# Kernel tuning notes

Measured on AMD Instinct MI355X. Metric: run time of the kernel, lower is better.

The kernel has to match this reference:

```python
import jax, jax.numpy as jnp
import numpy as np

B = 16; Hp = 24; Wp = 24; N = Hp * Wp + 2  # 578 = patches + cls + freq tokens
D = 768; H = 12; HDIM = D // H
BAND = 64; SD = 16  # sd = min(16, max(4, band_dim))
HID = 3072  # int(embed_dim * mlp_ratio)
SCALE = HDIM ** -0.5; CLIP = 10.0
FILM_SCALE = 0.5; SPEC_INIT = 0.02; GATE_INIT = 0.05


def _ln(x, w, b, eps=1e-6):
    m = jnp.mean(x, axis=-1, keepdims=True)
    v = jnp.mean((x - m) ** 2, axis=-1, keepdims=True)
    return (x - m) * jax.lax.rsqrt(v + eps) * w + b


def _rms(x, eps=1e-6):
    return x * jax.lax.rsqrt(jnp.mean(x * x, axis=-1, keepdims=True) + eps)


def setup_inputs() -> dict:
    key = jax.random.key(0)
    ks = jax.random.split(key, 16)
    rn = lambda k, s, sc=1.0: jax.random.normal(k, s, dtype=jnp.float32) * sc
    return {
        "x": rn(ks[0], (B, N, D)),
        "band_tokens": rn(ks[1], (B, 1, D)),  # unused by forward (matches torch signature)
        "freq_token_for_cond": rn(ks[2], (B, 1, D)),
        "freq_summary": rn(ks[3], (B, D)),
        "token_band_feat": rn(ks[4], (B, N, BAND)),
        "alpha": jnp.ones((1,), jnp.float32),
        "ln_gate_w": jnp.ones((D,), jnp.float32), "ln_gate_b": jnp.zeros((D,), jnp.float32),
        "film_w": rn(ks[5], (D, 2 * D), 1e-4), "film_b": jnp.zeros((2 * D,), jnp.float32),
        "ln_attn_w": jnp.ones((D,), jnp.float32), "ln_attn_b": jnp.zeros((D,), jnp.float32),
        "qkv_w": rn(ks[6], (D, 3 * D), 0.02), "qkv_b": jnp.zeros((3 * D,), jnp.float32),
        "proj_w": rn(ks[7], (D, D), 0.02), "proj_b": jnp.zeros((D,), jnp.float32),
        "spec_bias_scale": jnp.float32(SPEC_INIT),
        "gate_w": rn(ks[8], (D, H), 1e-4), "gate_b": jnp.zeros((H,), jnp.float32),
        "band_proj_w": rn(ks[9], (BAND, SD), 0.02),
        "ln_mlp_w": jnp.ones((D,), jnp.float32), "ln_mlp_b": jnp.zeros((D,), jnp.float32),
        "fc1_w": rn(ks[10], (D, HID), 0.02), "fc1_b": jnp.zeros((HID,), jnp.float32),
        "fc2_w": rn(ks[11], (HID, D), 0.02), "fc2_b": jnp.zeros((D,), jnp.float32),
        "dw_w": rn(ks[12], (HID, 1, 3, 3), 0.1), "dw_b": jnp.zeros((HID,), jnp.float32),
    }


def _forward(x, band_tokens, freq_token_for_cond, freq_summary, token_band_feat, alpha,
             ln_gate_w, ln_gate_b, film_w, film_b, ln_attn_w, ln_attn_b,
             qkv_w, qkv_b, proj_w, proj_b, spec_bias_scale, gate_w, gate_b, band_proj_w,
             ln_mlp_w, ln_mlp_b, fc1_w, fc1_b, fc2_w, fc2_b, dw_w, dw_b):
    a = alpha.reshape(())
    # --- FiLM gate on patch tokens (replaces patch, no residual) ---
    cls_freq = x[:, :2]
    patch = x[:, 2:]
    p = _ln(patch, ln_gate_w, ln_gate_b)
    gb = freq_summary @ film_w + film_b            # [B, 2D]
    gamma, beta = jnp.split(gb, 2, axis=-1)
    gamma = jnp.tanh(gamma) * FILM_SCALE
    beta = jnp.tanh(beta) * FILM_SCALE
    patch = p * (1.0 + a * gamma[:, None, :]) + a * beta[:, None, :]
    x = jnp.concatenate([cls_freq, patch], axis=1)
    # --- spectral-similarity attention ---
    xn = _ln(x, ln_attn_w, ln_attn_b)
    qkv = (xn @ qkv_w + qkv_b).reshape(B, N, 3, H, HDIM)
    q = _rms(qkv[:, :, 0].transpose(0, 2, 1, 3))   # [B,H,N,hd]
    k = _rms(qkv[:, :, 1].transpose(0, 2, 1, 3))
    v = qkv[:, :, 2].transpose(0, 2, 1, 3)
    logits = jnp.einsum('bhnd,bhmd->bhnm', q * SCALE, k)
    s = _rms(token_band_feat @ band_proj_w)        # [B,N,SD]
    ssim = jnp.einsum('bns,bms->bnm', s, s)        # [B,N,N]
    logits = jnp.clip(logits + a * spec_bias_scale * ssim[:, None], -CLIP, CLIP)
    attn = jax.nn.softmax(logits, axis=-1)
    out = jnp.einsum('bhnm,bhmd->bhnd', attn, v)
    g = jnp.tanh(freq_token_for_cond[:, 0] @ gate_w + gate_b) * GATE_INIT  # [B,H]
    out = out * (1.0 + a * g[:, :, None, None])
    out = out.transpose(0, 2, 1, 3).reshape(B, N, D)
    x = x + (out @ proj_w + proj_b)
    # --- conv MLP on patch tokens only ---
    cls_freq = x[:, :2]
    patch = x[:, 2:]
    h = jax.nn.gelu(_ln(patch, ln_mlp_w, ln_mlp_b) @ fc1_w + fc1_b, approximate=False)
    h = h.transpose(0, 2, 1).reshape(B, HID, Hp, Wp)
    h = jax.lax.conv_general_dilated(h, dw_w, (1, 1), 'SAME', feature_group_count=HID,
                                     dimension_numbers=('NCHW', 'OIHW', 'NCHW'))
    h = jax.nn.silu(h + dw_b[None, :, None, None])
    h = h.reshape(B, HID, Hp * Wp).transpose(0, 2, 1)
    patch = patch + (h @ fc2_w + fc2_b)
    return jnp.concatenate([cls_freq, patch], axis=1)


def reference(x, band_tokens, freq_token_for_cond, freq_summary, token_band_feat, alpha,
              ln_gate_w, ln_gate_b, film_w, film_b, ln_attn_w, ln_attn_b,
              qkv_w, qkv_b, proj_w, proj_b, spec_bias_scale, gate_w, gate_b, band_proj_w,
              ln_mlp_w, ln_mlp_b, fc1_w, fc1_b, fc2_w, fc2_b, dw_w, dw_b):
    return _forward(x, band_tokens, freq_token_for_cond, freq_summary, token_band_feat, alpha,
                    ln_gate_w, ln_gate_b, film_w, film_b, ln_attn_w, ln_attn_b,
                    qkv_w, qkv_b, proj_w, proj_b, spec_bias_scale, gate_w, gate_b, band_proj_w,
                    ln_mlp_w, ln_mlp_b, fc1_w, fc1_b, fc2_w, fc2_b, dw_w, dw_b)
```

## Files before the change

### kernel.cpp

```cpp
#include <hip/hip_runtime.h>
#include <hip/hip_bf16.h>

#define BATCH 16
#define NTOK 578
#define NTOKP 592
#define NP 576
#define PGRID 24
#define DIM 768
#define NH 12
#define HDIM 64
#define BAND 64
#define SDIM 16
#define HID 3072
#define SCALE 0.125f
#define CLIPV 10.0f
#define KHS 104
#define VTS 72
#define PLS 72

typedef __attribute__((ext_vector_type(8))) short bf16x8;
typedef __attribute__((ext_vector_type(4))) float f32x4;

__device__ __forceinline__ float b2f(short u) {
  union { float f; unsigned int i; } x;
  x.i = ((unsigned int)(unsigned short)u) << 16;
  return x.f;
}
__device__ __forceinline__ short f2b(float x) {
  __hip_bfloat16 h = __float2bfloat16(x);
  return *reinterpret_cast<short*>(&h);
}

__device__ __forceinline__ void gload16(const short* g, short* l) {
  __builtin_amdgcn_global_load_lds(
      (const __attribute__((address_space(1))) unsigned int*)g,
      (__attribute__((address_space(3))) unsigned int*)l, 16, 0, 0);
}

__device__ __forceinline__ int swz_wgid(int orig, int nwg) {
  int xcd = orig & 7, i = orig >> 3;
  int q = nwg >> 3, r = nwg & 7;
  return (xcd < r) ? xcd * (q + 1) + i : r * (q + 1) + (xcd - r) * q + i;
}

__device__ __forceinline__ void block_reduce2(float& a, float& b) {
  __shared__ float sm[8];
  #pragma unroll
  for (int o = 32; o > 0; o >>= 1) { a += __shfl_down(a, o); b += __shfl_down(b, o); }
  int lane = threadIdx.x & 63, w = threadIdx.x >> 6;
  __syncthreads();
  if (lane == 0) { sm[w] = a; sm[4 + w] = b; }
  __syncthreads();
  a = sm[0] + sm[1] + sm[2] + sm[3];
  b = sm[4] + sm[5] + sm[6] + sm[7];
}

__device__ __forceinline__ void tw_body(
    const float* __restrict__ W, short* __restrict__ Wt, int K, int N,
    int kblk, int nblk, float (*t)[33]) {
  int k0 = kblk * 32, n0 = nblk * 32;
  int tx = threadIdx.x & 31, ty = threadIdx.x >> 5;
  #pragma unroll
  for (int i = 0; i < 4; i++)
    t[ty + 8 * i][tx] = W[(size_t)(k0 + ty + 8 * i) * N + n0 + tx];
  __syncthreads();
  #pragma unroll
  for (int i = 0; i < 4; i++)
    Wt[(size_t)(n0 + ty + 8 * i) * K + k0 + tx] = f2b(t[tx][ty + 8 * i]);
}

__global__ __launch_bounds__(256) void prep_weights(
    const float* __restrict__ qkv_w, const float* __restrict__ proj_w,
    const float* __restrict__ fc1_w, const float* __restrict__ fc2_w,
    const float* __restrict__ dww,
    short* __restrict__ qkvT, short* __restrict__ projT,
    short* __restrict__ fc1T, short* __restrict__ fc2T, float* __restrict__ dwt) {
  __shared__ float t[32][33];
  int id = blockIdx.x;
  if (id < 1728) {
    tw_body(qkv_w, qkvT, 768, 2304, id % 24, id / 24, t);
  } else if (id < 2304) {
    int u = id - 1728; tw_body(proj_w, projT, 768, 768, u % 24, u / 24, t);
  } else if (id < 4608) {
    int u = id - 2304; tw_body(fc1_w, fc1T, 768, 3072, u % 24, u / 24, t);
  } else if (id < 6912) {
    int u = id - 4608; tw_body(fc2_w, fc2T, 3072, 768, u % 96, u / 96, t);
  } else {
    int i = (id - 6912) * 256 + threadIdx.x;
    if (i < 9 * HID) { int tt = i / HID, c = i - tt * HID; dwt[i] = dww[c * 9 + tt]; }
  }
}

__global__ __launch_bounds__(256) void transpose_v(
    const short* __restrict__ v, short* __restrict__ vT) {
  __shared__ short t[64][72];
  int bh = blockIdx.y;
  int n0 = blockIdx.x * 64;
  int tid = threadIdx.x;
  const short* vb = v + (size_t)bh * NTOK * HDIM;
  short* ob = vT + (size_t)bh * HDIM * NTOKP;
  {
    int r = tid >> 2, c0 = (tid & 3) * 16;
    int n = n0 + r;
    bf16x8 a0 = {0,0,0,0,0,0,0,0}, a1 = {0,0,0,0,0,0,0,0};
    if (n < NTOK) {
      a0 = *(const bf16x8*)(vb + (size_t)n * HDIM + c0);
      a1 = *(const bf16x8*)(vb + (size_t)n * HDIM + c0 + 8);
    }
    *(bf16x8*)(&t[r][c0]) = a0;
    *(bf16x8*)(&t[r][c0 + 8]) = a1;
  }
  __syncthreads();
  {
    int d = tid & 63, nc = tid >> 6;
    int nbase = n0 + nc * 16;
    short tmp[16];
    #pragma unroll
    for (int e = 0; e < 16; e++) tmp[e] = t[nc * 16 + e][d];
    if (nbase + 16 <= NTOK) {
      *(bf16x8*)(ob + (size_t)d * NTOKP + nbase) = *(bf16x8*)tmp;
      *(bf16x8*)(ob + (size_t)d * NTOKP + nbase + 8) = *(bf16x8*)(tmp + 8);
    } else {
      for (int e = 0; e < 16; e++)
        if (nbase + e < NTOK) ob[(size_t)d * NTOKP + nbase + e] = tmp[e];
    }
  }
}

__global__ __launch_bounds__(256) void film_kernel(
    const float* __restrict__ fsum, const float* __restrict__ film_w, const float* __restrict__ film_b,
    const float* __restrict__ ftc, const float* __restrict__ gate_w, const float* __restrict__ gate_b,
    float* __restrict__ gamma, float* __restrict__ beta, float* __restrict__ g) {
  int idx = blockIdx.x * 256 + threadIdx.x;
  const int TOT_FILM = BATCH * 2 * DIM;
  if (idx < TOT_FILM) {
    int b = idx / (2 * DIM), col = idx % (2 * DIM);
    float acc = film_b[col];
    for (int i = 0; i < DIM; i++) acc += fsum[b * DIM + i] * film_w[(size_t)i * 2 * DIM + col];
    float t = tanhf(acc) * 0.5f;
    if (col < DIM) gamma[b * DIM + col] = t; else beta[b * DIM + (col - DIM)] = t;
  } else if (idx < TOT_FILM + BATCH * NH) {
    int i2 = idx - TOT_FILM;
    int b = i2 / NH, h = i2 % NH;
    float acc = gate_b[h];
    for (int i = 0; i < DIM; i++) acc += ftc[b * DIM + i] * gate_w[i * NH + h];
    g[i2] = tanhf(acc) * 0.05f;
  }
}

__global__ __launch_bounds__(256) void ln_film_kernel(
    const float* __restrict__ x, const float* __restrict__ gamma, const float* __restrict__ beta,
    const float* __restrict__ gw, const float* __restrict__ gb,
    const float* __restrict__ aw, const float* __restrict__ ab,
    const float* __restrict__ alpha, float* __restrict__ xw, __hip_bfloat16* __restrict__ xn) {
  int row = blockIdx.x;
  int b = row / NTOK, n = row % NTOK;
  int tid = threadIdx.x;
  const float* xr = x + (size_t)row * DIM;
  float vals[3];
  #pragma unroll
  for (int j = 0; j < 3; j++) vals[j] = xr[tid + j * 256];
  if (n >= 2) {
    float s = vals[0] + vals[1] + vals[2];
    float ss = vals[0]*vals[0] + vals[1]*vals[1] + vals[2]*vals[2];
    block_reduce2(s, ss);
    float mean = s * (1.f / 768.f);
    float inv = rsqrtf(ss * (1.f / 768.f) - mean * mean + 1e-6f);
    float a = alpha[0];
    #pragma unroll
    for (int j = 0; j < 3; j++) {
      int d = tid + j * 256;
      float p = (vals[j] - mean) * inv * gw[d] + gb[d];
      vals[j] = p * (1.f + a * gamma[(size_t)b * DIM + d]) + a * beta[(size_t)b * DIM + d];
    }
  }
  float* xwr = xw + (size_t)row * DIM;
  #pragma unroll
  for (int j = 0; j < 3; j++) xwr[tid + j * 256] = vals[j];
  float s = vals[0] + vals[1] + vals[2];
  float ss = vals[0]*vals[0] + vals[1]*vals[1] + vals[2]*vals[2];
  block_reduce2(s, ss);
  float mean = s * (1.f / 768.f);
  float inv = rsqrtf(ss * (1.f / 768.f) - mean * mean + 1e-6f);
  __hip_bfloat16* xnr = xn + (size_t)row * DIM;
  #pragma unroll
  for (int j = 0; j < 3; j++) {
    int d = tid + j * 256;
    xnr[d] = __float2bfloat16((vals[j] - mean) * inv * aw[d] + ab[d]);
  }
}

__global__ __launch_bounds__(256) void band_s_kernel(
    const float* __restrict__ tbf, const float* __restrict__ bw, float* __restrict__ s) {
  int row = blockIdx.x * 4 + (threadIdx.x >> 6);
  int lane = threadIdx.x & 63;
  if (row >= BATCH * NTOK) return;
  const float* t = tbf + (size_t)row * BAND;
  float val = 0.f;
  if (lane < SDIM) {
    for (int i = 0; i < BAND; i++) val += t[i] * bw[i * SDIM + lane];
  }
  float ss = val * val;
  #pragma unroll
  for (int o = 8; o > 0; o >>= 1) ss += __shfl_xor(ss, o, 16);
  if (lane < SDIM) s[(size_t)row * SDIM + lane] = val * rsqrtf(ss * (1.f / 16.f) + 1e-6f);
}

__device__ __forceinline__ void stage_tile(
    const short* __restrict__ A, const short* __restrict__ Wt, int K,
    int m0, int n0, int kt, short* Al, short* Bl, int wid, int lrow, int lcol) {
  #pragma unroll
  for (int it = 0; it < 4; it++) {
    int r0 = wid * 8 + it * 32;
    gload16(A + (size_t)(m0 + r0 + lrow) * K + kt + lcol, Al + r0 * 64);
    gload16(Wt + (size_t)(n0 + r0 + lrow) * K + kt + lcol, Bl + r0 * 64);
  }
}

__device__ __forceinline__ void compute_tile(
    const short* Al, const short* Bl, f32x4 acc[4][4],
    int wr, int wc, int ln15, int kb) {
  #pragma unroll
  for (int kk = 0; kk < 2; kk++) {
    bf16x8 af[4], bfr[4];
    #pragma unroll
    for (int i = 0; i < 4; i++)
      af[i] = *(const bf16x8*)(Al + (wr * 64 + i * 16 + ln15) * 64 + kk * 32 + kb * 8);
    #pragma unroll
    for (int j = 0; j < 4; j++)
      bfr[j] = *(const bf16x8*)(Bl + (wc * 64 + j * 16 + ln15) * 64 + kk * 32 + kb * 8);
    #pragma unroll
    for (int i = 0; i < 4; i++)
      #pragma unroll
      for (int j = 0; j < 4; j++)
        acc[i][j] = __builtin_amdgcn_mfma_f32_16x16x32_bf16(af[i], bfr[j], acc[i][j], 0, 0, 0);
  }
}

__device__ __forceinline__ void mfma_core_g(
    const short* __restrict__ A, const short* __restrict__ Wt,
    int K, int m0, int n0, f32x4 acc[4][4],
    short* Al0, short* Bl0, short* Al1, short* Bl1) {
  int tid = threadIdx.x, lane = tid & 63, wid = tid >> 6;
  int wr = wid >> 1, wc = wid & 1;
  int ln15 = lane & 15, kb = lane >> 4;
  int lrow = lane >> 3, lcol = (lane & 7) * 8;
  #pragma unroll
  for (int i = 0; i < 4; i++)
    #pragma unroll
    for (int j = 0; j < 4; j++) acc[i][j] = (f32x4){0.f, 0.f, 0.f, 0.f};
  stage_tile(A, Wt, K, m0, n0, 0, Al0, Bl0, wid, lrow, lcol);
  __syncthreads();
  for (int kt = 0; kt < K; kt += 128) {
    if (kt + 64 < K)
      stage_tile(A, Wt, K, m0, n0, kt + 64, Al1, Bl1, wid, lrow, lcol);
    compute_tile(Al0, Bl0, acc, wr, wc, ln15, kb);
    __syncthreads();
    if (kt + 128 < K)
      stage_tile(A, Wt, K, m0, n0, kt + 128, Al0, Bl0, wid, lrow, lcol);
    if (kt + 64 < K)
      compute_tile(Al1, Bl1, acc, wr, wc, ln15, kb);
    __syncthreads();
  }
}

__device__ __forceinline__ void stage_tile64(
    const short* __restrict__ A, const short* __restrict__ Wt, int K,
    int m0, int n0, int kt, short* Al, short* Bl, int wid, int lrow, int lcol) {
  #pragma unroll
  for (int it = 0; it < 2; it++) {
    int r0 = wid * 8 + it * 32;
    gload16(A + (size_t)(m0 + r0 + lrow) * K + kt + lcol, Al + r0 * 64);
  }
  #pragma unroll
  for (int it = 0; it < 4; it++) {
    int r0 = wid * 8 + it * 32;
    gload16(Wt + (size_t)(n0 + r0 + lrow) * K + kt + lcol, Bl + r0 * 64);
  }
}

__device__ __forceinline__ void compute_tile64(
    const short* Al, const short* Bl, f32x4 acc[4][2],
    int wid, int ln15, int kb) {
  #pragma unroll
  for (int kk = 0; kk < 2; kk++) {
    bf16x8 af[4], bfr[2];
    #pragma unroll
    for (int i = 0; i < 4; i++)
      af[i] = *(const bf16x8*)(Al + (i * 16 + ln15) * 64 + kk * 32 + kb * 8);
    #pragma unroll
    for (int j = 0; j < 2; j++)
      bfr[j] = *(const bf16x8*)(Bl + (wid * 32 + j * 16 + ln15) * 64 + kk * 32 + kb * 8);
    #pragma unroll
    for (int i = 0; i < 4; i++)
      #pragma unroll
      for (int j = 0; j < 2; j++)
        acc[i][j] = __builtin_amdgcn_mfma_f32_16x16x32_bf16(af[i], bfr[j], acc[i][j], 0, 0, 0);
  }
}

__device__ __forceinline__ void mfma_core_64(
    const short* __restrict__ A, const short* __restrict__ Wt,
    int K, int m0, int n0, f32x4 acc[4][2],
    short* Al0, short* Bl0, short* Al1, short* Bl1) {
  int tid = threadIdx.x, lane = tid & 63, wid = tid >> 6;
  int ln15 = lane & 15, kb = lane >> 4;
  int lrow = lane >> 3, lcol = (lane & 7) * 8;
  #pragma unroll
  for (int i = 0; i < 4; i++)
    #pragma unroll
    for (int j = 0; j < 2; j++) acc[i][j] = (f32x4){0.f, 0.f, 0.f, 0.f};
  stage_tile64(A, Wt, K, m0, n0, 0, Al0, Bl0, wid, lrow, lcol);
  __syncthreads();
  for (int kt = 0; kt < K; kt += 128) {
    if (kt + 64 < K)
      stage_tile64(A, Wt, K, m0, n0, kt + 64, Al1, Bl1, wid, lrow, lcol);
    compute_tile64(Al0, Bl0, acc, wid, ln15, kb);
    __syncthreads();
    if (kt + 128 < K)
      stage_tile64(A, Wt, K, m0, n0, kt + 128, Al0, Bl0, wid, lrow, lcol);
    if (kt + 64 < K)
      compute_tile64(Al1, Bl1, acc, wid, ln15, kb);
    __syncthreads();
  }
}

__global__ __launch_bounds__(256) void gemm_qkv(
    const short* __restrict__ A, const short* __restrict__ Wt, const float* __restrict__ bias,
    __hip_bfloat16* __restrict__ q, __hip_bfloat16* __restrict__ k, __hip_bfloat16* __restrict__ v) {
  __shared__ short Al[2 * 128 * 64], Bl[2 * 128 * 64];
  f32x4 acc[4][4];
  int wgid = swz_wgid(blockIdx.x, 18 * 73);
  int m0 = (wgid / 18) * 128, n0 = (wgid % 18) * 128;
  mfma_core_g(A, Wt, DIM, m0, n0, acc, Al, Bl, Al + 128 * 64, Bl + 128 * 64);
  int tid = threadIdx.x, lane = tid & 63, wid = tid >> 6, wr = wid >> 1, wc = wid & 1;
  int ln15 = lane & 15, lq = lane >> 4;
  int colbase = n0 + wc * 64;
  int which = colbase / DIM;
  int rem = colbase - which * DIM;
  int h = rem >> 6;
  __hip_bfloat16* dst = (which == 0) ? q : ((which == 1) ? k : v);
  float fin_scale = (which == 0) ? SCALE : 1.0f;
  float bv[4];
  #pragma unroll
  for (int j = 0; j < 4; j++) bv[j] = bias[colbase + j * 16 + ln15];
  #pragma unroll
  for (int i = 0; i < 4; i++) {
    #pragma unroll
    for (int r = 0; r < 4; r++) {
      int m = m0 + wr * 64 + i * 16 + lq * 4 + r;
      float v4[4];
      #pragma unroll
      for (int j = 0; j < 4; j++) v4[j] = acc[i][j][r] + bv[j];
      float inv = fin_scale;
      if (which < 2) {
        float ss = v4[0]*v4[0] + v4[1]*v4[1] + v4[2]*v4[2] + v4[3]*v4[3];
        ss += __shfl_xor(ss, 1); ss += __shfl_xor(ss, 2);
        ss += __shfl_xor(ss, 4); ss += __shfl_xor(ss, 8);
        inv = rsqrtf(ss * (1.f / 64.f) + 1e-6f) * fin_scale;
      }
      if (m < BATCH * NTOK) {
        int b = m / NTOK, n = m - b * NTOK;
        __hip_bfloat16* orow = dst + (((size_t)b * NH + h) * NTOK + n) * HDIM;
        #pragma unroll
        for (int j = 0; j < 4; j++)
          orow[j * 16 + ln15] = __float2bfloat16(v4[j] * inv);
      }
    }
  }
}

__global__ __launch_bounds__(512) void attn_mfma(
    const short* __restrict__ q, const short* __restrict__ k,
    const short* __restrict__ vT, const float* __restrict__ s,
    const float* __restrict__ g, const float* __restrict__ alpha,
    const float* __restrict__ sbs, short* __restrict__ ao) {
  __shared__ short Kh[2][64 * KHS];
  __shared__ short Vt[2][64 * VTS];
  __shared__ short Pl[8][16 * PLS];
  int xcd = blockIdx.x & 7, idx = blockIdx.x >> 3;
  int bh = xcd * 24 + idx / 5;
  int n0 = (idx % 5) * 128;
  int b = bh / NH, h = bh - b * NH;
  int tid = threadIdx.x, lane = tid & 63, w = tid >> 6;
  int l15 = lane & 15, lg = lane >> 4;
  float a = alpha[0], c = a * sbs[0];
  const short* qb = q + (size_t)bh * NTOK * HDIM;
  const short* kb = k + (size_t)bh * NTOK * HDIM;
  const short* vtb = vT + (size_t)bh * HDIM * NTOKP;
  const float* sb = s + (size_t)b * NTOK * SDIM;
  const bf16x8 Z8 = {0, 0, 0, 0, 0, 0, 0, 0};

  int qrow = n0 + w * 16 + l15;
  int qsrc = (qrow < NTOK) ? qrow : 0;
  bf16x8 qf0 = *(const bf16x8*)(qb + (size_t)qsrc * HDIM + lg * 8);
  bf16x8 qf1 = *(const bf16x8*)(qb + (size_t)qsrc * HDIM + 32 + lg * 8);
  bf16x8 qf2 = Z8;
  if (lg < 2) {
    const float* sp = sb + (size_t)qsrc * SDIM + lg * 8;
    #pragma unroll
    for (int j = 0; j < 8; j++) qf2[j] = f2b(c * sp[j]);
  }

  f32x4 accO[4];
  #pragma unroll
  for (int dd = 0; dd < 4; dd++) accO[dd] = (f32x4){0.f, 0.f, 0.f, 0.f};
  float rsum[4] = {0.f, 0.f, 0.f, 0.f};

  int srow = (tid & 255) >> 2, sseg = tid & 3;
  if (tid < 256 && sseg == 3) {
    #pragma unroll
    for (int bb = 0; bb < 2; bb++) {
      short* dst = Kh[bb] + srow * KHS + 80;
      *(bf16x8*)dst = Z8;
      *(bf16x8*)(dst + 8) = Z8;
    }
  }

  auto stage = [&](int mt, short* KhB, short* VtB) {
    if (tid < 256) {
      int key = mt + srow;
      bool kok = key < NTOK;
      if (sseg < 2) {
        bf16x8 v0 = Z8, v1 = Z8, v2 = Z8, v3 = Z8;
        if (kok) {
          const short* src = kb + (size_t)key * HDIM + sseg * 32;
          v0 = *(const bf16x8*)(src);
          v1 = *(const bf16x8*)(src + 8);
          v2 = *(const bf16x8*)(src + 16);
          v3 = *(const bf16x8*)(src + 24);
        }
        short* dst = KhB + srow * KHS + sseg * 32;
        *(bf16x8*)dst = v0;
        *(bf16x8*)(dst + 8) = v1;
        *(bf16x8*)(dst + 16) = v2;
        *(bf16x8*)(dst + 24) = v3;
      } else if (sseg == 2) {
        bf16x8 v0 = Z8, v1 = Z8;
        if (kok) {
          const float* sp = sb + (size_t)key * SDIM;
          #pragma unroll
          for (int j = 0; j < 8; j++) { v0[j] = f2b(sp[j]); v1[j] = f2b(sp[j + 8]); }
        }
        short* dst = KhB + srow * KHS + 64;
        *(bf16x8*)dst = v0;
        *(bf16x8*)(dst + 8) = v1;
      }
    } else {
      int kk0 = sseg * 16;
      short* dst = VtB + srow * VTS + kk0;
      const short* src = vtb + (size_t)srow * NTOKP + mt + kk0;
      if (mt + kk0 + 16 <= NTOK) {
        *(bf16x8*)dst = *(const bf16x8*)src;
        *(bf16x8*)(dst + 8) = *(const bf16x8*)(src + 8);
      } else {
        for (int e = 0; e < 16; e++)
          dst[e] = (mt + kk0 + e < NTOK) ? src[e] : (short)0;
      }
    }
  };

  stage(0, Kh[0], Vt[0]);
  __syncthreads();
  const int NT = 10;
  for (int ti = 0; ti < NT; ti++) {
    int mt = ti * 64, cur = ti & 1;
    if (ti + 1 < NT) stage(mt + 64, Kh[cur ^ 1], Vt[cur ^ 1]);
    const short* KhC = Kh[cur];
    const short* VtC = Vt[cur];
    f32x4 sa[4];
    __builtin_amdgcn_s_setprio(1);
    #pragma unroll
    for (int jj = 0; jj < 4; jj++) {
      sa[jj] = (f32x4){0.f, 0.f, 0.f, 0.f};
      const short* kp = KhC + (jj * 16 + l15) * KHS + lg * 8;
      sa[jj] = __builtin_amdgcn_mfma_f32_16x16x32_bf16(qf0, *(const bf16x8*)kp, sa[jj], 0, 0, 0);
      sa[jj] = __builtin_amdgcn_mfma_f32_16x16x32_bf16(qf1, *(const bf16x8*)(kp + 32), sa[jj], 0, 0, 0);
      sa[jj] = __builtin_amdgcn_mfma_f32_16x16x32_bf16(qf2, *(const bf16x8*)(kp + 64), sa[jj], 0, 0, 0);
    }
    __builtin_amdgcn_s_setprio(0);
    short* pw = Pl[w];
    float ps[4][4];
    #pragma unroll
    for (int jj = 0; jj < 4; jj++) {
      bool ok = (mt + jj * 16 + l15) < NTOK;
      #pragma unroll
      for (int r = 0; r < 4; r++) {
        float x = sa[jj][r];
        x = fminf(fmaxf(x, -CLIPV), CLIPV);
        float e = ok ? __expf(x) : 0.f;
        ps[jj][r] = e;
        pw[(lg * 4 + r) * PLS + jj * 16 + l15] = f2b(e);
      }
    }
    #pragma unroll
    for (int r = 0; r < 4; r++) {
      float t = ps[0][r] + ps[1][r] + ps[2][r] + ps[3][r];
      t += __shfl_xor(t, 1); t += __shfl_xor(t, 2);
      t += __shfl_xor(t, 4); t += __shfl_xor(t, 8);
      rsum[r] += t;
    }
    __builtin_amdgcn_s_setprio(1);
    #pragma unroll
    for (int kc = 0; kc < 2; kc++) {
      bf16x8 pa = *(const bf16x8*)(pw + l15 * PLS + kc * 32 + lg * 8);
      #pragma unroll
      for (int dd = 0; dd < 4; dd++) {
        bf16x8 vf = *(const bf16x8*)(VtC + (dd * 16 + l15) * VTS + kc * 32 + lg * 8);
        accO[dd] = __builtin_amdgcn_mfma_f32_16x16x32_bf16(pa, vf, accO[dd], 0, 0, 0);
      }
    }
    __builtin_amdgcn_s_setprio(0);
    __syncthreads();
  }
  float gm = 1.f + a * g[bh];
  #pragma unroll
  for (int r = 0; r < 4; r++) {
    int n = n0 + w * 16 + lg * 4 + r;
    if (n >= NTOK) continue;
    float inv = gm / rsum[r];
    short* orow = ao + ((size_t)b * NTOK + n) * DIM + h * HDIM;
    #pragma unroll
    for (int dd = 0; dd < 4; dd++)
      orow[dd * 16 + l15] = f2b(accO[dd][r] * inv);
  }
}

__global__ __launch_bounds__(256) void gemm_proj(
    const short* __restrict__ A, const short* __restrict__ Wt, const float* __restrict__ bias,
    float* __restrict__ xw, float* __restrict__ out) {
  __shared__ short Al[2 * 64 * 64], Bl[2 * 128 * 64];
  f32x4 acc[4][2];
  int wgid = swz_wgid(blockIdx.x, 145 * 6);
  int m0 = (wgid / 6) * 64, n0 = (wgid % 6) * 128;
  mfma_core_64(A, Wt, DIM, m0, n0, acc, Al, Bl, Al + 64 * 64, Bl + 128 * 64);
  int tid = threadIdx.x, lane = tid & 63, wid = tid >> 6;
  int ln15 = lane & 15, lq = lane >> 4;
  #pragma unroll
  for (int i = 0; i < 4; i++) {
    #pragma unroll
    for (int j = 0; j < 2; j++) {
      int col = n0 + wid * 32 + j * 16 + ln15;
      float bv = bias[col];
      #pragma unroll
      for (int r = 0; r < 4; r++) {
        int m = m0 + i * 16 + lq * 4 + r;
        if (m >= BATCH * NTOK) continue;
        int n = m % NTOK;
        float val = acc[i][j][r] + bv + xw[(size_t)m * DIM + col];
        xw[(size_t)m * DIM + col] = val;
        if (n < 2) out[(size_t)m * DIM + col] = val;
      }
    }
  }
}

__global__ __launch_bounds__(256) void ln_mlp_kernel(
    const float* __restrict__ x2, const float* __restrict__ w, const float* __restrict__ bb,
    __hip_bfloat16* __restrict__ xm) {
  int r = blockIdx.x;
  int b = r / NP, pi = r % NP;
  int tid = threadIdx.x;
  const float* xr = x2 + ((size_t)b * NTOK + 2 + pi) * DIM;
  float vals[3];
  #pragma unroll
  for (int j = 0; j < 3; j++) vals[j] = xr[tid + j * 256];
  float s = vals[0] + vals[1] + vals[2];
  float ss = vals[0]*vals[0] + vals[1]*vals[1] + vals[2]*vals[2];
  block_reduce2(s, ss);
  float mean = s * (1.f / 768.f);
  float inv = rsqrtf(ss * (1.f / 768.f) - mean * mean + 1e-6f);
  __hip_bfloat16* xo = xm + (size_t)r * DIM;
  #pragma unroll
  for (int j = 0; j < 3; j++) {
    int d = tid + j * 256;
    xo[d] = __float2bfloat16((vals[j] - mean) * inv * w[d] + bb[d]);
  }
}

__global__ __launch_bounds__(256) void gemm_fc1(
    const short* __restrict__ A, const short* __restrict__ Wt, const float* __restrict__ bias,
    __hip_bfloat16* __restrict__ h1) {
  __shared__ short Al[2 * 128 * 64], Bl[2 * 128 * 64];
  f32x4 acc[4][4];
  int wgid = swz_wgid(blockIdx.x, 24 * 36);
  int m0 = (wgid / 24) * 128, n0 = (wgid % 24) * 128;
  mfma_core_g(A, Wt, DIM, m0, n0, acc, Al, Bl, Al + 128 * 64, Bl + 128 * 64);
  int tid = threadIdx.x, lane = tid & 63, wid = tid >> 6, wr = wid >> 1, wc = wid & 1;
  int ln15 = lane & 15, lq = lane >> 4;
  #pragma unroll
  for (int i = 0; i < 4; i++) {
    #pragma unroll
    for (int j = 0; j < 4; j++) {
      int col = n0 + wc * 64 + j * 16 + ln15;
      float bv = bias[col];
      #pragma unroll
      for (int r = 0; r < 4; r++) {
        int m = m0 + wr * 64 + i * 16 + lq * 4 + r;
        float val = acc[i][j][r] + bv;
        float ge = 0.5f * val * (1.f + erff(val * 0.70710678118f));
        h1[(size_t)m * HID + col] = __float2bfloat16(ge);
      }
    }
  }
}

__global__ __launch_bounds__(256) void dwconv_kernel(
    const __hip_bfloat16* __restrict__ h1, const float* __restrict__ dwt,
    const float* __restrict__ dwb, __hip_bfloat16* __restrict__ h2) {
  int gx = blockIdx.x;
  int b = gx / 144, g = gx - b * 144;
  int y = g / 6, x0 = (g - y * 6) * 4;
  int tid = threadIdx.x;
  int c0 = blockIdx.y * 512 + (tid & 63) * 8;
  int x = x0 + (tid >> 6);
  const short* in = (const short*)h1 + (size_t)b * NP * HID + c0;
  bf16x8 iv[3][3];
  #pragma unroll
  for (int ky = 0; ky < 3; ky++) {
    int yy = y + ky - 1;
    #pragma unroll
    for (int kx = 0; kx < 3; kx++) {
      int xx = x + kx - 1;
      bool ok = (yy >= 0 && yy < PGRID && xx >= 0 && xx < PGRID);
      iv[ky][kx] = ok ? *(const bf16x8*)(in + (size_t)(yy * PGRID + xx) * HID)
                      : (bf16x8){0, 0, 0, 0, 0, 0, 0, 0};
    }
  }
  float acc[8];
  {
    float4 b0 = *(const float4*)(dwb + c0);
    float4 b1 = *(const float4*)(dwb + c0 + 4);
    acc[0] = b0.x; acc[1] = b0.y; acc[2] = b0.z; acc[3] = b0.w;
    acc[4] = b1.x; acc[5] = b1.y; acc[6] = b1.z; acc[7] = b1.w;
  }
  #pragma unroll
  for (int t = 0; t < 9; t++) {
    float4 w0 = *(const float4*)(dwt + t * HID + c0);
    float4 w1 = *(const float4*)(dwt + t * HID + c0 + 4);
    bf16x8 xv = iv[t / 3][t % 3];
    acc[0] += b2f(xv[0]) * w0.x; acc[1] += b2f(xv[1]) * w0.y;
    acc[2] += b2f(xv[2]) * w0.z; acc[3] += b2f(xv[3]) * w0.w;
    acc[4] += b2f(xv[4]) * w1.x; acc[5] += b2f(xv[5]) * w1.y;
    acc[6] += b2f(xv[6]) * w1.z; acc[7] += b2f(xv[7]) * w1.w;
  }
  short ov[8];
  #pragma unroll
  for (int e = 0; e < 8; e++) {
    float v = acc[e];
    ov[e] = f2b(v / (1.f + __expf(-v)));
  }
  *(bf16x8*)((short*)h2 + ((size_t)b * NP + y * PGRID + x) * HID + c0) = *(bf16x8*)ov;
}

__global__ __launch_bounds__(256) void gemm_fc2(
    const short* __restrict__ A, const short* __restrict__ Wt, const float* __restrict__ bias,
    const float* __restrict__ xw, float* __restrict__ out, int b0) {
  __shared__ short Al[2 * 64 * 64], Bl[2 * 128 * 64];
  f32x4 acc[4][2];
  int wgid = swz_wgid(blockIdx.x, 72 * 6);
  int m0 = (wgid / 6) * 64, n0 = (wgid % 6) * 128;
  mfma_core_64(A, Wt, HID, m0, n0, acc, Al, Bl, Al + 64 * 64, Bl + 128 * 64);
  int tid = threadIdx.x, lane = tid & 63, wid = tid >> 6;
  int ln15 = lane & 15, lq = lane >> 4;
  #pragma unroll
  for (int i = 0; i < 4; i++) {
    #pragma unroll
    for (int j = 0; j < 2; j++) {
      int col = n0 + wid * 32 + j * 16 + ln15;
      float bv = bias[col];
      #pragma unroll
      for (int r = 0; r < 4; r++) {
        int m = m0 + i * 16 + lq * 4 + r;
        int bl = m / NP, pi = m - bl * NP;
        size_t orow = ((size_t)(b0 + bl) * NTOK + 2 + pi) * DIM;
        out[orow + col] = acc[i][j][r] + bv + xw[orow + col];
      }
    }
  }
}

extern "C" void kernel_launch(void* const* d_in, const int* in_sizes, int n_in,
                              void* d_out, int out_size, void* d_ws, size_t ws_size,
                              hipStream_t stream) {
  const float* x      = (const float*)d_in[0];
  const float* ftc    = (const float*)d_in[2];
  const float* fsum   = (const float*)d_in[3];
  const float* tbf    = (const float*)d_in[4];
  const float* alpha  = (const float*)d_in[5];
  const float* lgw    = (const float*)d_in[6];
  const float* lgb    = (const float*)d_in[7];
  const float* film_w = (const float*)d_in[8];
  const float* film_b = (const float*)d_in[9];
  const float* law    = (const float*)d_in[10];
  const float* lab    = (const float*)d_in[11];
  const float* qkv_w  = (const float*)d_in[12];
  const float* qkv_b  = (const float*)d_in[13];
  const float* proj_w = (const float*)d_in[14];
  const float* proj_b = (const float*)d_in[15];
  const float* sbs    = (const float*)d_in[16];
  const float* gate_w = (const float*)d_in[17];
  const float* gate_b = (const float*)d_in[18];
  const float* band_w = (const float*)d_in[19];
  const float* lmw    = (const float*)d_in[20];
  const float* lmb    = (const float*)d_in[21];
  const float* fc1_w  = (const float*)d_in[22];
  const float* fc1_b  = (const float*)d_in[23];
  const float* fc2_w  = (const float*)d_in[24];
  const float* fc2_b  = (const float*)d_in[25];
  const float* dw_w   = (const float*)d_in[26];
  const float* dw_b   = (const float*)d_in[27];
  float* out = (float*)d_out;

  float* ws = (float*)d_ws;
  const size_t SZ = (size_t)BATCH * NTOK * DIM;

  float* p_xw = ws;
  short* p_xn = (short*)(ws + SZ);
  short* p_q  = (short*)(ws + SZ + SZ / 2);
  short* p_k  = (short*)(ws + 2 * SZ);
  short* p_v  = (short*)(ws + 2 * SZ + SZ / 2);
  float* p_s  = ws + 3 * SZ;
  float* p_gamma = p_s + (size_t)BATCH * NTOK * SDIM;
  float* p_beta  = p_gamma + BATCH * DIM;
  float* p_g     = p_beta + BATCH * DIM;
  float* p_dwt   = p_g + 256;
  float* wtb = p_dwt + 9 * HID;
  short* qkvT = (short*)wtb;
  short* projT = qkvT + (size_t)768 * 2304;
  short* fc1T  = projT + (size_t)768 * 768;
  short* fc2T  = fc1T + (size_t)768 * 3072;
  short* h2c   = fc2T + (size_t)3072 * 768;

  const size_t total_floats =
      3 * SZ + (size_t)BATCH * NTOK * SDIM + 2 * (size_t)BATCH * DIM + 256 + 9 * HID +
      ((size_t)768 * 2304 + 768 * 768 + 768 * 3072 + 3072 * 768) / 2 +
      ((size_t)8 * NP * HID) / 2;
  if (ws_size < total_floats * sizeof(float)) return;

  short* p_ao = p_xn;
  short* p_xm = p_q;
  short* h1c  = p_k;
  short* p_vT = h2c;

  dim3 blk(256);

  prep_weights<<<dim3(7020), blk, 0, stream>>>(
      qkv_w, proj_w, fc1_w, fc2_w, dw_w, qkvT, projT, fc1T, fc2T, p_dwt);

  film_kernel<<<dim3((BATCH * 2 * DIM + BATCH * NH + 255) / 256), blk, 0, stream>>>(
      fsum, film_w, film_b, ftc, gate_w, gate_b, p_gamma, p_beta, p_g);

  ln_film_kernel<<<dim3(BATCH * NTOK), blk, 0, stream>>>(
      x, p_gamma, p_beta, lgw, lgb, law, lab, alpha, p_xw, (__hip_bfloat16*)p_xn);

  band_s_kernel<<<dim3((BATCH * NTOK + 3) / 4), blk, 0, stream>>>(tbf, band_w, p_s);

  gemm_qkv<<<dim3(18 * 73), blk, 0, stream>>>(
      p_xn, qkvT, qkv_b, (__hip_bfloat16*)p_q, (__hip_bfloat16*)p_k, (__hip_bfloat16*)p_v);

  transpose_v<<<dim3(10, BATCH * NH), blk, 0, stream>>>(p_v, p_vT);

  attn_mfma<<<dim3(960), dim3(512), 0, stream>>>(
      p_q, p_k, p_vT, p_s, p_g, alpha, sbs, p_ao);

  gemm_proj<<<dim3(145 * 6), blk, 0, stream>>>(p_ao, projT, proj_b, p_xw, out);

  ln_mlp_kernel<<<dim3(BATCH * NP), blk, 0, stream>>>(p_xw, lmw, lmb, (__hip_bfloat16*)p_xm);

  for (int cc = 0; cc < 2; cc++) {
    const short* Ach = p_xm + (size_t)cc * 4608 * DIM;
    gemm_fc1<<<dim3(24 * 36), blk, 0, stream>>>(Ach, fc1T, fc1_b, (__hip_bfloat16*)h1c);
    dwconv_kernel<<<dim3(8 * 144, 6), blk, 0, stream>>>(
        (const __hip_bfloat16*)h1c, p_dwt, dw_b, (__hip_bfloat16*)h2c);
    gemm_fc2<<<dim3(72 * 6), blk, 0, stream>>>(h2c, fc2T, fc2_b, p_xw, out, cc * 8);
  }
}
```

Baseline: 527.6 us.

## Use 256x128 single-buffered GEMM tiles for QKV and FC1; batch FiLM matvec via LDS

QKV and FC1 GEMMs now launch 512-thread blocks computing 256x128 output tiles, with 8 waves sharing one staged B tile. The old double-buffered pipeline is replaced by a simple stage/sync/compute/sync loop. The aim is to raise arithmetic intensity per staged byte and reduce the block count, at the cost of losing load/compute overlap. The film kernel is also restructured so each block caches fsum in LDS and each thread accumulates four batches per weight load, cutting redundant film_w reads.

Result: no change. 517.3 us (-2.0%).

```diff
diff --git a/kernel.cpp b/kernel.cpp
--- a/kernel.cpp
+++ b/kernel.cpp
@@ -131,20 +131,37 @@
     const float* __restrict__ fsum, const float* __restrict__ film_w, const float* __restrict__ film_b,
     const float* __restrict__ ftc, const float* __restrict__ gate_w, const float* __restrict__ gate_b,
     float* __restrict__ gamma, float* __restrict__ beta, float* __restrict__ g) {
-  int idx = blockIdx.x * 256 + threadIdx.x;
-  const int TOT_FILM = BATCH * 2 * DIM;
-  if (idx < TOT_FILM) {
-    int b = idx / (2 * DIM), col = idx % (2 * DIM);
-    float acc = film_b[col];
-    for (int i = 0; i < DIM; i++) acc += fsum[b * DIM + i] * film_w[(size_t)i * 2 * DIM + col];
-    float t = tanhf(acc) * 0.5f;
-    if (col < DIM) gamma[b * DIM + col] = t; else beta[b * DIM + (col - DIM)] = t;
-  } else if (idx < TOT_FILM + BATCH * NH) {
-    int i2 = idx - TOT_FILM;
-    int b = i2 / NH, h = i2 % NH;
-    float acc = gate_b[h];
-    for (int i = 0; i < DIM; i++) acc += ftc[b * DIM + i] * gate_w[i * NH + h];
-    g[i2] = tanhf(acc) * 0.05f;
+  int bid = blockIdx.x, tid = threadIdx.x;
+  if (bid < 24) {
+    __shared__ float fs[BATCH][DIM];
+    for (int i = tid; i < BATCH * DIM; i += 256) fs[i / DIM][i - (i / DIM) * DIM] = fsum[i];
+    __syncthreads();
+    int col = bid * 64 + (tid & 63);
+    int b0 = tid >> 6;
+    float acc[4];
+    float bv = film_b[col];
+    #pragma unroll
+    for (int i = 0; i < 4; i++) acc[i] = bv;
+    for (int k = 0; k < DIM; k++) {
+      float w = film_w[(size_t)k * 2 * DIM + col];
+      #pragma unroll
+      for (int i = 0; i < 4; i++) acc[i] += fs[b0 + 4 * i][k] * w;
+    }
+    #pragma unroll
+    for (int i = 0; i < 4; i++) {
+      int b = b0 + 4 * i;
+      float t = tanhf(acc[i]) * 0.5f;
+      if (col < DIM) gamma[b * DIM + col] = t;
+      else beta[b * DIM + (col - DIM)] = t;
+    }
+  } else {
+    int i2 = tid;
+    if (i2 < BATCH * NH) {
+      int b = i2 / NH, h = i2 - b * NH;
+      float acc = gate_b[h];
+      for (int i = 0; i < DIM; i++) acc += ftc[b * DIM + i] * gate_w[i * NH + h];
+      g[i2] = tanhf(acc) * 0.05f;
+    }
   }
 }
 
@@ -206,6 +223,60 @@
   if (lane < SDIM) s[(size_t)row * SDIM + lane] = val * rsqrtf(ss * (1.f / 16.f) + 1e-6f);
 }
 
+__device__ __forceinline__ void stage_tile256(
+    const short* __restrict__ A, const short* __restrict__ Wt, int K,
+    int m0, int n0, int kt, short* Al, short* Bl, int wid, int lrow, int lcol) {
+  #pragma unroll
+  for (int it = 0; it < 4; it++) {
+    int r0 = wid * 8 + it * 64;
+    gload16(A + (size_t)(m0 + r0 + lrow) * K + kt + lcol, Al + r0 * 64);
+  }
+  #pragma unroll
+  for (int it = 0; it < 2; it++) {
+    int r0 = wid * 8 + it * 64;
+    gload16(Wt + (size_t)(n0 + r0 + lrow) * K + kt + lcol, Bl + r0 * 64);
+  }
+}
+
+__device__ __forceinline__ void compute_tile256(
+    const short* Al, const short* Bl, f32x4 acc[4][4],
+    int wr, int wc, int ln15, int kb) {
+  #pragma unroll
+  for (int kk = 0; kk < 2; kk++) {
+    bf16x8 af[4], bfr[4];
+    #pragma unroll
+    for (int i = 0; i < 4; i++)
+      af[i] = *(const bf16x8*)(Al + (wr * 64 + i * 16 + ln15) * 64 + kk * 32 + kb * 8);
+    #pragma unroll
+    for (int j = 0; j < 4; j++)
+      bfr[j] = *(const bf16x8*)(Bl + (wc * 64 + j * 16 + ln15) * 64 + kk * 32 + kb * 8);
+    #pragma unroll
+    for (int i = 0; i < 4; i++)
+      #pragma unroll
+      for (int j = 0; j < 4; j++)
+        acc[i][j] = __builtin_amdgcn_mfma_f32_16x16x32_bf16(af[i], bfr[j], acc[i][j], 0, 0, 0);
+  }
+}
+
+__device__ __forceinline__ void mfma_core_256(
+    const short* __restrict__ A, const short* __restrict__ Wt,
+    int K, int m0, int n0, f32x4 acc[4][4], short* Al, short* Bl) {
+  int tid = threadIdx.x, lane = tid & 63, wid = tid >> 6;
+  int wr = wid >> 1, wc = wid & 1;
+  int ln15 = lane & 15, kb = lane >> 4;
+  int lrow = lane >> 3, lcol = (lane & 7) * 8;
+  #pragma unroll
+  for (int i = 0; i < 4; i++)
+    #pragma unroll
+    for (int j = 0; j < 4; j++) acc[i][j] = (f32x4){0.f, 0.f, 0.f, 0.f};
+  for (int kt = 0; kt < K; kt += 64) {
+    stage_tile256(A, Wt, K, m0, n0, kt, Al, Bl, wid, lrow, lcol);
+    __syncthreads();
+    compute_tile256(Al, Bl, acc, wr, wc, ln15, kb);
+    __syncthreads();
+  }
+}
+
 __device__ __forceinline__ void stage_tile(
     const short* __restrict__ A, const short* __restrict__ Wt, int K,
     int m0, int n0, int kt, short* Al, short* Bl, int wid, int lrow, int lcol) {
@@ -214,53 +285,6 @@
     int r0 = wid * 8 + it * 32;
     gload16(A + (size_t)(m0 + r0 + lrow) * K + kt + lcol, Al + r0 * 64);
     gload16(Wt + (size_t)(n0 + r0 + lrow) * K + kt + lcol, Bl + r0 * 64);
-  }
-}
-
-__device__ __forceinline__ void compute_tile(
-    const short* Al, const short* Bl, f32x4 acc[4][4],
-    int wr, int wc, int ln15, int kb) {
-  #pragma unroll
-  for (int kk = 0; kk < 2; kk++) {
-    bf16x8 af[4], bfr[4];
-    #pragma unroll
-    for (int i = 0; i < 4; i++)
-      af[i] = *(const bf16x8*)(Al + (wr * 64 + i * 16 + ln15) * 64 + kk * 32 + kb * 8);
-    #pragma unroll
-    for (int j = 0; j < 4; j++)
-      bfr[j] = *(const bf16x8*)(Bl + (wc * 64 + j * 16 + ln15) * 64 + kk * 32 + kb * 8);
-    #pragma unroll
-    for (int i = 0; i < 4; i++)
-      #pragma unroll
-      for (int j = 0; j < 4; j++)
-        acc[i][j] = __builtin_amdgcn_mfma_f32_16x16x32_bf16(af[i], bfr[j], acc[i][j], 0, 0, 0);
-  }
-}
-
-__device__ __forceinline__ void mfma_core_g(
-    const short* __restrict__ A, const short* __restrict__ Wt,
-    int K, int m0, int n0, f32x4 acc[4][4],
-    short* Al0, short* Bl0, short* Al1, short* Bl1) {
-  int tid = threadIdx.x, lane = tid & 63, wid = tid >> 6;
-  int wr = wid >> 1, wc = wid & 1;
-  int ln15 = lane & 15, kb = lane >> 4;
-  int lrow = lane >> 3, lcol = (lane & 7) * 8;
-  #pragma unroll
-  for (int i = 0; i < 4; i++)
-    #pragma unroll
-    for (int j = 0; j < 4; j++) acc[i][j] = (f32x4){0.f, 0.f, 0.f, 0.f};
-  stage_tile(A, Wt, K, m0, n0, 0, Al0, Bl0, wid, lrow, lcol);
-  __syncthreads();
-  for (int kt = 0; kt < K; kt += 128) {
-    if (kt + 64 < K)
-      stage_tile(A, Wt, K, m0, n0, kt + 64, Al1, Bl1, wid, lrow, lcol);
-    compute_tile(Al0, Bl0, acc, wr, wc, ln15, kb);
-    __syncthreads();
-    if (kt + 128 < K)
-      stage_tile(A, Wt, K, m0, n0, kt + 128, Al0, Bl0, wid, lrow, lcol);
-    if (kt + 64 < K)
-      compute_tile(Al1, Bl1, acc, wr, wc, ln15, kb);
-    __syncthreads();
   }
 }
 
@@ -325,14 +349,14 @@
   }
 }
 
-__global__ __launch_bounds__(256) void gemm_qkv(
+__global__ __launch_bounds__(512) void gemm_qkv(
     const short* __restrict__ A, const short* __restrict__ Wt, const float* __restrict__ bias,
     __hip_bfloat16* __restrict__ q, __hip_bfloat16* __restrict__ k, __hip_bfloat16* __restrict__ v) {
-  __shared__ short Al[2 * 128 * 64], Bl[2 * 128 * 64];
+  __shared__ short Al[256 * 64], Bl[128 * 64];
   f32x4 acc[4][4];
-  int wgid = swz_wgid(blockIdx.x, 18 * 73);
-  int m0 = (wgid / 18) * 128, n0 = (wgid % 18) * 128;
-  mfma_core_g(A, Wt, DIM, m0, n0, acc, Al, Bl, Al + 128 * 64, Bl + 128 * 64);
+  int wgid = swz_wgid(blockIdx.x, 37 * 18);
+  int m0 = (wgid / 18) * 256, n0 = (wgid % 18) * 128;
+  mfma_core_256(A, Wt, DIM, m0, n0, acc, Al, Bl);
   int tid = threadIdx.x, lane = tid & 63, wid = tid >> 6, wr = wid >> 1, wc = wid & 1;
   int ln15 = lane & 15, lq = lane >> 4;
   int colbase = n0 + wc * 64;
@@ -578,14 +602,14 @@
   }
 }
 
-__global__ __launch_bounds__(256) void gemm_fc1(
+__global__ __launch_bounds__(512) void gemm_fc1(
     const short* __restrict__ A, const short* __restrict__ Wt, const float* __restrict__ bias,
     __hip_bfloat16* __restrict__ h1) {
-  __shared__ short Al[2 * 128 * 64], Bl[2 * 128 * 64];
+  __shared__ short Al[256 * 64], Bl[128 * 64];
   f32x4 acc[4][4];
-  int wgid = swz_wgid(blockIdx.x, 24 * 36);
-  int m0 = (wgid / 24) * 128, n0 = (wgid % 24) * 128;
-  mfma_core_g(A, Wt, DIM, m0, n0, acc, Al, Bl, Al + 128 * 64, Bl + 128 * 64);
+  int wgid = swz_wgid(blockIdx.x, 18 * 24);
+  int m0 = (wgid / 24) * 256, n0 = (wgid % 24) * 128;
+  mfma_core_256(A, Wt, DIM, m0, n0, acc, Al, Bl);
   int tid = threadIdx.x, lane = tid & 63, wid = tid >> 6, wr = wid >> 1, wc = wid & 1;
   int ln15 = lane & 15, lq = lane >> 4;
   #pragma unroll
@@ -748,7 +772,7 @@
   prep_weights<<<dim3(7020), blk, 0, stream>>>(
       qkv_w, proj_w, fc1_w, fc2_w, dw_w, qkvT, projT, fc1T, fc2T, p_dwt);
 
-  film_kernel<<<dim3((BATCH * 2 * DIM + BATCH * NH + 255) / 256), blk, 0, stream>>>(
+  film_kernel<<<dim3(25), blk, 0, stream>>>(
       fsum, film_w, film_b, ftc, gate_w, gate_b, p_gamma, p_beta, p_g);
 
   ln_film_kernel<<<dim3(BATCH * NTOK), blk, 0, stream>>>(
@@ -756,7 +780,7 @@
 
   band_s_kernel<<<dim3((BATCH * NTOK + 3) / 4), blk, 0, stream>>>(tbf, band_w, p_s);
 
-  gemm_qkv<<<dim3(18 * 73), blk, 0, stream>>>(
+  gemm_qkv<<<dim3(37 * 18), dim3(512), 0, stream>>>(
       p_xn, qkvT, qkv_b, (__hip_bfloat16*)p_q, (__hip_bfloat16*)p_k, (__hip_bfloat16*)p_v);
 
   transpose_v<<<dim3(10, BATCH * NH), blk, 0, stream>>>(p_v, p_vT);
@@ -770,7 +794,7 @@
 
   for (int cc = 0; cc < 2; cc++) {
     const short* Ach = p_xm + (size_t)cc * 4608 * DIM;
-    gemm_fc1<<<dim3(24 * 36), blk, 0, stream>>>(Ach, fc1T, fc1_b, (__hip_bfloat16*)h1c);
+    gemm_fc1<<<dim3(18 * 24), dim3(512), 0, stream>>>(Ach, fc1T, fc1_b, (__hip_bfloat16*)h1c);
     dwconv_kernel<<<dim3(8 * 144, 6), blk, 0, stream>>>(
         (const __hip_bfloat16*)h1c, p_dwt, dw_b, (__hip_bfloat16*)h2c);
     gemm_fc2<<<dim3(72 * 6), blk, 0, stream>>>(h2c, fc2T, fc2_b, p_xw, out, cc * 8);
```
